# Kernel tuning notes

Measured on AMD Instinct MI355X. Metric: run time of the kernel, lower is better.

## Reference

```python
import jax, jax.numpy as jnp
import numpy as np

DIM_EMB = 1024
DIM_K = 128
DIM_V = 128
BATCH = 4
SEQ = 4096

def setup_inputs() -> dict:
    key = jax.random.key(0)
    kx, kq, kk, kv = jax.random.split(key, 4)
    x = jax.random.normal(kx, (BATCH, SEQ, DIM_EMB), dtype=jnp.float32)
    Wq = jax.random.normal(kq, (DIM_EMB, DIM_K), dtype=jnp.float32) * (1.0 / np.sqrt(DIM_EMB))
    Wk = jax.random.normal(kk, (DIM_EMB, DIM_K), dtype=jnp.float32) * (1.0 / np.sqrt(DIM_EMB))
    Wv = jax.random.normal(kv, (DIM_EMB, DIM_V), dtype=jnp.float32) * (1.0 / np.sqrt(DIM_EMB))
    return {"x": x, "Wq": Wq, "Wk": Wk, "Wv": Wv}

def reference(x, Wq, Wk, Wv):
    # x: [b, s, e]; projections (torch Linear without bias -> x @ W)
    seq_len = x.shape[1]
    q = x @ Wq  # [b, s, dk]
    k = x @ Wk  # [b, s, dk]
    v = x @ Wv  # [b, s, dv]
    # NOTE: original scales by 1/sqrt(dim_emb), not 1/sqrt(dim_k)
    scale = 1.0 / np.sqrt(x.shape[-1])
    qk = jnp.einsum('bqd,bkd->bqk', q, k) * scale  # [b, s, s]
    causal = jnp.tril(jnp.ones((seq_len, seq_len), dtype=bool))
    masked_qk = jnp.where(causal, qk, -jnp.inf)
    att = jax.nn.softmax(masked_qk, axis=-1)  # dropout p=0.0 -> identity
    return att @ v  # [b, s, dv]
```

## Files before the change

### kernel.cpp

```cpp
#include <hip/hip_runtime.h>

typedef __attribute__((ext_vector_type(8))) short s8v;
typedef __attribute__((ext_vector_type(4))) short s4v;
typedef __attribute__((ext_vector_type(4))) float f4v;

#define S_ 4096
#define E_ 1024
#define D_ 128

__device__ __forceinline__ unsigned short f2bf(float f) {
  unsigned int u = __float_as_uint(f);
  return (unsigned short)((u + 0x7FFFu + ((u >> 16) & 1u)) >> 16);
}

__device__ __forceinline__ unsigned int cvtpk(float lo, float hi) {
  unsigned int r;
  asm("v_cvt_pk_bf16_f32 %0, %1, %2" : "=v"(r) : "v"(lo), "v"(hi));
  return r;
}

__device__ __forceinline__ void gload16(const void* g, void* l) {
  __builtin_amdgcn_global_load_lds(
      (const __attribute__((address_space(1))) unsigned int*)g,
      (__attribute__((address_space(3))) unsigned int*)l, 16, 0, 0);
}

__device__ __forceinline__ int slot_off(int s) { return s * (3840 - 256 * s); }

__global__ __launch_bounds__(256) void prep_kernel(
    const float* __restrict__ Wq, const float* __restrict__ Wk,
    const float* __restrict__ Wv, unsigned short* __restrict__ Wt) {
  __shared__ unsigned short T[64][72];
  const int w = blockIdx.x;
  const int p = w >> 5, bx = w & 31;
  const float* W = (p == 0) ? Wq : (p == 1) ? Wk : Wv;
  const int k0 = (bx >> 1) * 64;
  const int n0 = (bx & 1) * 64;
  const int t = threadIdx.x, rr = t >> 4, c4 = (t & 15) * 4;
#pragma unroll
  for (int i = 0; i < 4; ++i) {
    int kr = i * 16 + rr;
    float4 ww = *reinterpret_cast<const float4*>(W + (size_t)(k0 + kr) * D_ + n0 + c4);
    T[c4 + 0][kr] = f2bf(ww.x); T[c4 + 1][kr] = f2bf(ww.y);
    T[c4 + 2][kr] = f2bf(ww.z); T[c4 + 3][kr] = f2bf(ww.w);
  }
  __syncthreads();
#pragma unroll
  for (int i = 0; i < 4; ++i) {
    int n = i * 16 + rr;
    s4v v;
    v[0] = (short)T[n][c4]; v[1] = (short)T[n][c4 + 1];
    v[2] = (short)T[n][c4 + 2]; v[3] = (short)T[n][c4 + 3];
    *reinterpret_cast<s4v*>(Wt + (size_t)(p * D_ + n0 + n) * E_ + k0 + c4) = v;
  }
}

__global__ __launch_bounds__(256, 3) void proj_kernel(
    const float* __restrict__ x, const unsigned short* __restrict__ Wt,
    unsigned short* __restrict__ Qb, unsigned short* __restrict__ Kb,
    unsigned short* __restrict__ VT) {
  __shared__ __align__(16) unsigned short As[2][128 * 64];
  __shared__ __align__(16) unsigned short Bs[2][64 * 64];
  const int bid = blockIdx.x;
  const int cls = bid & 7, j = bid >> 3;
  const int m0 = (cls * 16 + j / 6) * 128, ng = j % 6;
  const int t = threadIdx.x;
  const int wv = t >> 6, lane = t & 63, quad = lane >> 4, l16 = lane & 15;
  const int wr = wv >> 1, wc = wv & 1;

  f4v acc[4][2];
  const f4v fz = {0.f, 0.f, 0.f, 0.f};
#pragma unroll
  for (int i = 0; i < 4; ++i)
#pragma unroll
    for (int k = 0; k < 2; ++k) acc[i][k] = fz;

  const int ar = t >> 1, khalf = t & 1;
  const float* xg = x + (size_t)(m0 + ar) * E_ + khalf * 32;

  const int lrow = lane >> 3;
  const int scb = ((lane & 7) ^ lrow) * 16;
  const char* bSrc = (const char*)(Wt + (size_t)(ng * 64 + wv * 16 + lrow) * E_) + scb;

  const int xm = (l16 & 7) * 16;

  float4 xa[8];
#pragma unroll
  for (int m = 0; m < 8; ++m) xa[m] = *reinterpret_cast<const float4*>(xg + 4 * m);
#pragma unroll
  for (int i = 0; i < 2; ++i)
    gload16(bSrc + (size_t)(i * 8 * E_) * 2, (char*)Bs[0] + wv * 2048 + i * 1024);

  int buf = 0;
  for (int kk = 0; kk < E_; kk += 64, buf ^= 1) {
#pragma unroll
    for (int j2 = 0; j2 < 4; ++j2) {
      union { unsigned int u[4]; s8v v; } gv;
      gv.u[0] = cvtpk(xa[2 * j2].x, xa[2 * j2].y);
      gv.u[1] = cvtpk(xa[2 * j2].z, xa[2 * j2].w);
      gv.u[2] = cvtpk(xa[2 * j2 + 1].x, xa[2 * j2 + 1].y);
      gv.u[3] = cvtpk(xa[2 * j2 + 1].z, xa[2 * j2 + 1].w);
      const int g = khalf * 4 + j2;
      *reinterpret_cast<s8v*>((char*)As[buf] + ar * 128 + ((g ^ (ar & 7)) * 16)) = gv.v;
    }
    __syncthreads();
    if (kk + 64 < E_) {
#pragma unroll
      for (int m = 0; m < 8; ++m)
        xa[m] = *reinterpret_cast<const float4*>(xg + kk + 64 + 4 * m);
#pragma unroll
      for (int i = 0; i < 2; ++i)
        gload16(bSrc + (size_t)(i * 8 * E_ + kk + 64) * 2,
                (char*)Bs[buf ^ 1] + wv * 2048 + i * 1024);
    }
    const char* Ab = (const char*)As[buf] + (wr * 64 + l16) * 128;
    const char* Bb = (const char*)Bs[buf] + (wc * 32 + l16) * 128;
#pragma unroll
    for (int ks = 0; ks < 2; ++ks) {
      const int co = (ks * 64 + quad * 16) ^ xm;
      s8v af[4], bf[2];
#pragma unroll
      for (int rt = 0; rt < 4; ++rt)
        af[rt] = *reinterpret_cast<const s8v*>(Ab + rt * 2048 + co);
#pragma unroll
      for (int ct = 0; ct < 2; ++ct)
        bf[ct] = *reinterpret_cast<const s8v*>(Bb + ct * 2048 + co);
#pragma unroll
      for (int rt = 0; rt < 4; ++rt)
#pragma unroll
        for (int ct = 0; ct < 2; ++ct)
          acc[rt][ct] = __builtin_amdgcn_mfma_f32_16x16x32_bf16(
              af[rt], bf[ct], acc[rt][ct], 0, 0, 0);
    }
  }

  const int p = ng >> 1, n0 = (ng & 1) * 64;
  if (p < 2) {
    unsigned short* dst = p ? Kb : Qb;
#pragma unroll
    for (int rt = 0; rt < 4; ++rt)
#pragma unroll
      for (int ct = 0; ct < 2; ++ct)
#pragma unroll
        for (int r = 0; r < 4; ++r)
          dst[(size_t)(m0 + wr * 64 + rt * 16 + quad * 4 + r) * D_ +
              n0 + wc * 32 + ct * 16 + l16] = f2bf(acc[rt][ct][r]);
  } else {
    const int b = m0 >> 12;
    const int s0 = (m0 & (S_ - 1)) + wr * 64;
#pragma unroll
    for (int rt = 0; rt < 4; ++rt)
#pragma unroll
      for (int ct = 0; ct < 2; ++ct) {
        s4v v;
        v[0] = (short)f2bf(acc[rt][ct][0]); v[1] = (short)f2bf(acc[rt][ct][1]);
        v[2] = (short)f2bf(acc[rt][ct][2]); v[3] = (short)f2bf(acc[rt][ct][3]);
        *reinterpret_cast<s4v*>(
            VT + ((size_t)b * D_ + n0 + wc * 32 + ct * 16 + l16) * S_ + s0 +
            rt * 16 + quad * 4) = v;
      }
  }
}

__global__ __launch_bounds__(256, 5) void flash_kernel(
    const unsigned short* __restrict__ Qb, const unsigned short* __restrict__ Kb,
    const unsigned short* __restrict__ VT, float* __restrict__ Op,
    float* __restrict__ Lp) {
  __shared__ __align__(16) unsigned short KS[64 * 128];
  __shared__ __align__(16) unsigned short VS[128 * 64];
  const int id = blockIdx.x;
  const int xcd = id & 7;
  const int b = xcd >> 1;
  const int sub = 287 - ((id >> 3) * 2 + (xcd & 1));
  int g = 0;
#pragma unroll
  for (int gg = 0; gg < 7; ++gg)
    if (sub >= 4 * (gg + 1) * (gg + 2)) g = gg + 1;
  const int off = sub - 4 * g * (g + 1);
  const int qt = 8 * g + off / (g + 1);
  const int s = off % (g + 1);
  const int q0 = qt * 64;
  const int klo = s * 512;
  const int khi = min((s + 1) * 512, (qt + 1) * 64);

  const int t = threadIdx.x;
  const int wv = t >> 6, lane = t & 63, quad = lane >> 4, l16 = lane & 15;
  const int qrow0 = q0 + wv * 16;
  const float SCL2 = 0.03125f * 1.44269504088896340736f;

  const unsigned short* Kbb = Kb + (size_t)b * S_ * D_;
  const unsigned short* Vbb = VT + (size_t)b * D_ * S_;

  s8v Qf[4];
#pragma unroll
  for (int ks = 0; ks < 4; ++ks)
    Qf[ks] = *reinterpret_cast<const s8v*>(
        Qb + ((size_t)b * S_ + qrow0 + l16) * D_ + ks * 32 + quad * 8);

  f4v O[8];
  const f4v fz = {0.f, 0.f, 0.f, 0.f};
#pragma unroll
  for (int nt = 0; nt < 8; ++nt) O[nt] = fz;
  float lt = 0.f;

  for (int k0 = klo; k0 < khi; k0 += 64) {
    __syncthreads();
#pragma unroll
    for (int i = 0; i < 4; ++i) {
      const int ci = wv * 4 + i;
      const int kr = ci * 4 + (lane >> 4);
      const int sg = (kr & 3) | (((((kr >> 3) & 1) + 2 * (kr >> 4)) & 3) << 2);
      gload16(Kbb + (size_t)(k0 + kr) * D_ + (((lane & 15) ^ sg) * 8),
              (char*)KS + ci * 1024);
      const int dv = ci * 8 + (lane >> 3);
      gload16(Vbb + (size_t)dv * S_ + k0 + (((lane & 7) ^ (dv & 7)) * 8),
              (char*)VS + ci * 1024);
    }
    __syncthreads();

    if (k0 <= qrow0 + 15) {
      f4v St[2][2];
#pragma unroll
      for (int c = 0; c < 2; ++c)
#pragma unroll
        for (int s2 = 0; s2 < 2; ++s2) St[c][s2] = fz;
      __builtin_amdgcn_s_setprio(1);
#pragma unroll
      for (int ks = 0; ks < 4; ++ks)
#pragma unroll
        for (int c = 0; c < 2; ++c)
#pragma unroll
          for (int s2 = 0; s2 < 2; ++s2) {
            const int row = c * 32 + ((l16 >> 2) << 3) + s2 * 4 + (l16 & 3);
            s8v kf = *reinterpret_cast<const s8v*>(
                KS + row * 128 + (((ks * 4 + quad) ^ l16) * 8));
            St[c][s2] = __builtin_amdgcn_mfma_f32_16x16x32_bf16(
                kf, Qf[ks], St[c][s2], 0, 0, 0);
          }
      __builtin_amdgcn_s_setprio(0);
      const bool full = (k0 + 63 <= qrow0);
      s8v pf[2];
#pragma unroll
      for (int c = 0; c < 2; ++c) {
        float e[8];
        float ladd = 0.f;
#pragma unroll
        for (int s2 = 0; s2 < 2; ++s2)
#pragma unroll
          for (int r = 0; r < 4; ++r) {
            float ev = exp2f(St[c][s2][r] * SCL2);
            if (!full) {
              int key = k0 + c * 32 + quad * 8 + s2 * 4 + r;
              if (key > qrow0 + l16) ev = 0.f;
            }
            e[s2 * 4 + r] = ev;
            ladd += ev;
          }
        lt += ladd;
        union { unsigned int u[4]; s8v v; } P;
        P.u[0] = cvtpk(e[0], e[1]); P.u[1] = cvtpk(e[2], e[3]);
        P.u[2] = cvtpk(e[4], e[5]); P.u[3] = cvtpk(e[6], e[7]);
        pf[c] = P.v;
      }
      __builtin_amdgcn_s_setprio(1);
#pragma unroll
      for (int c = 0; c < 2; ++c)
#pragma unroll
        for (int nt = 0; nt < 8; ++nt) {
          s8v vf = *reinterpret_cast<const s8v*>(
              (const char*)VS + (nt * 16 + l16) * 128 +
              (((c * 4 + quad) ^ (l16 & 7)) * 16));
          O[nt] = __builtin_amdgcn_mfma_f32_16x16x32_bf16(
              pf[c], vf, O[nt], 0, 0, 0);
        }
      __builtin_amdgcn_s_setprio(0);
    }
  }

  lt += __shfl_xor(lt, 16);
  lt += __shfl_xor(lt, 32);
  const int soff = slot_off(s);
#pragma unroll
  for (int nt = 0; nt < 8; ++nt)
#pragma unroll
    for (int r = 0; r < 4; ++r)
      Op[((size_t)(qrow0 + quad * 4 + r + soff) * 4 + b) * D_ + nt * 16 + l16] =
          O[nt][r];
  if (lane < 16) Lp[(size_t)(qrow0 + l16 + soff) * 4 + b] = lt;
}

__global__ __launch_bounds__(256) void norm_kernel(
    const float* __restrict__ Op, const float* __restrict__ Lp,
    float* __restrict__ out) {
  const int idx = blockIdx.x * 256 + threadIdx.x;
  const int rowg = idx >> 5, d4 = idx & 31;
  const int b = rowg >> 12, row = rowg & 4095;
  const int g = row >> 9;
  float ax = 0.f, ay = 0.f, az = 0.f, aw = 0.f, L = 0.f;
  for (int s = 0; s <= g; ++s) {
    const size_t pr = (size_t)(row + slot_off(s)) * 4 + b;
    float4 o = reinterpret_cast<const float4*>(Op + pr * D_)[d4];
    ax += o.x; ay += o.y; az += o.z; aw += o.w;
    L += Lp[pr];
  }
  float4 r;
  const float inv = 1.f / L;
  r.x = ax * inv; r.y = ay * inv; r.z = az * inv; r.w = aw * inv;
  reinterpret_cast<float4*>(out)[idx] = r;
}

extern "C" void kernel_launch(void* const* d_in, const int* in_sizes, int n_in,
                              void* d_out, int out_size, void* d_ws, size_t ws_size,
                              hipStream_t stream) {
  const float* x = (const float*)d_in[0];
  const float* Wq = (const float*)d_in[1];
  const float* Wk = (const float*)d_in[2];
  const float* Wv = (const float*)d_in[3];
  float* out = (float*)d_out;

  char* ws = (char*)d_ws;
  unsigned short* Qb = (unsigned short*)ws;
  unsigned short* Kb = (unsigned short*)(ws + (((size_t)4) << 20));
  unsigned short* VT = (unsigned short*)(ws + (((size_t)8) << 20));
  unsigned short* Wt = (unsigned short*)(ws + (((size_t)12) << 20));
  float* Op = (float*)(ws + (((size_t)13) << 20));
  float* Lp = (float*)(ws + (((size_t)50) << 20));

  prep_kernel<<<96, 256, 0, stream>>>(Wq, Wk, Wv, Wt);
  proj_kernel<<<768, 256, 0, stream>>>(x, Wt, Qb, Kb, VT);
  flash_kernel<<<1152, 256, 0, stream>>>(Qb, Kb, VT, Op, Lp);
  norm_kernel<<<2048, 256, 0, stream>>>(Op, Lp, out);
}
```

Before: 204.5 us.

## Load fp32 x directly to LDS in projection; register-prefetch K/V in flash kernel

The projection kernel now streams fp32 x tiles straight into LDS with direct global-to-LDS loads and converts to bf16 while reading MFMA fragments. This replaces the register-staged, double-buffered bf16 A tile with a single fp32 buffer, and occupancy hints rise to 4 blocks per CU. The flash kernel swaps direct global-to-LDS K/V loads for register prefetching of the next tile during compute, and raises its occupancy hint to 8. The projection loses its double buffering, so load latency is hidden only by other resident blocks, and the flash kernel now uses more registers for the prefetch.

New measurement: 186.6 us. 8.8% less time.

```diff
diff --git a/kernel.cpp b/kernel.cpp
--- a/kernel.cpp
+++ b/kernel.cpp
@@ -55,12 +55,12 @@
   }
 }
 
-__global__ __launch_bounds__(256, 3) void proj_kernel(
+__global__ __launch_bounds__(256, 4) void proj_kernel(
     const float* __restrict__ x, const unsigned short* __restrict__ Wt,
     unsigned short* __restrict__ Qb, unsigned short* __restrict__ Kb,
     unsigned short* __restrict__ VT) {
-  __shared__ __align__(16) unsigned short As[2][128 * 64];
-  __shared__ __align__(16) unsigned short Bs[2][64 * 64];
+  __shared__ __align__(16) float Asf[128 * 64];
+  __shared__ __align__(16) unsigned short Bsb[64 * 64];
   const int bid = blockIdx.x;
   const int cls = bid & 7, j = bid >> 3;
   const int m0 = (cls * 16 + j / 6) * 128, ng = j % 6;
@@ -75,53 +75,42 @@
 #pragma unroll
     for (int k = 0; k < 2; ++k) acc[i][k] = fz;
 
-  const int ar = t >> 1, khalf = t & 1;
-  const float* xg = x + (size_t)(m0 + ar) * E_ + khalf * 32;
-
+  const char* aSrc0 =
+      (const char*)(x + (size_t)(m0 + wv * 32 + (lane >> 4)) * E_);
   const int lrow = lane >> 3;
   const int scb = ((lane & 7) ^ lrow) * 16;
   const char* bSrc = (const char*)(Wt + (size_t)(ng * 64 + wv * 16 + lrow) * E_) + scb;
 
-  const int xm = (l16 & 7) * 16;
-
-  float4 xa[8];
-#pragma unroll
-  for (int m = 0; m < 8; ++m) xa[m] = *reinterpret_cast<const float4*>(xg + 4 * m);
-#pragma unroll
-  for (int i = 0; i < 2; ++i)
-    gload16(bSrc + (size_t)(i * 8 * E_) * 2, (char*)Bs[0] + wv * 2048 + i * 1024);
-
-  int buf = 0;
-  for (int kk = 0; kk < E_; kk += 64, buf ^= 1) {
-#pragma unroll
-    for (int j2 = 0; j2 < 4; ++j2) {
-      union { unsigned int u[4]; s8v v; } gv;
-      gv.u[0] = cvtpk(xa[2 * j2].x, xa[2 * j2].y);
-      gv.u[1] = cvtpk(xa[2 * j2].z, xa[2 * j2].w);
-      gv.u[2] = cvtpk(xa[2 * j2 + 1].x, xa[2 * j2 + 1].y);
-      gv.u[3] = cvtpk(xa[2 * j2 + 1].z, xa[2 * j2 + 1].w);
-      const int g = khalf * 4 + j2;
-      *reinterpret_cast<s8v*>((char*)As[buf] + ar * 128 + ((g ^ (ar & 7)) * 16)) = gv.v;
-    }
+  const char* Ab = (const char*)Asf + (size_t)(wr * 64 + l16) * 256;
+  const char* Bb = (const char*)Bsb + (wc * 32 + l16) * 128;
+
+  for (int kk = 0; kk < E_; kk += 64) {
+#pragma unroll
+    for (int i = 0; i < 8; ++i) {
+      const int gsrc = (lane & 15) ^ ((i * 4 + (lane >> 4)) & 15);
+      gload16(aSrc0 + (size_t)i * 16384 + kk * 4 + gsrc * 16,
+              (char*)Asf + wv * 8192 + i * 1024);
+    }
+#pragma unroll
+    for (int i = 0; i < 2; ++i)
+      gload16(bSrc + (size_t)(i * 8 * E_ + kk) * 2, (char*)Bsb + wv * 2048 + i * 1024);
     __syncthreads();
-    if (kk + 64 < E_) {
-#pragma unroll
-      for (int m = 0; m < 8; ++m)
-        xa[m] = *reinterpret_cast<const float4*>(xg + kk + 64 + 4 * m);
-#pragma unroll
-      for (int i = 0; i < 2; ++i)
-        gload16(bSrc + (size_t)(i * 8 * E_ + kk + 64) * 2,
-                (char*)Bs[buf ^ 1] + wv * 2048 + i * 1024);
-    }
-    const char* Ab = (const char*)As[buf] + (wr * 64 + l16) * 128;
-    const char* Bb = (const char*)Bs[buf] + (wc * 32 + l16) * 128;
 #pragma unroll
     for (int ks = 0; ks < 2; ++ks) {
-      const int co = (ks * 64 + quad * 16) ^ xm;
       s8v af[4], bf[2];
-#pragma unroll
-      for (int rt = 0; rt < 4; ++rt)
-        af[rt] = *reinterpret_cast<const s8v*>(Ab + rt * 2048 + co);
+      const int g0 = ks * 8 + quad * 2;
+#pragma unroll
+      for (int rt = 0; rt < 4; ++rt) {
+        float4 a0 = *reinterpret_cast<const float4*>(
+            Ab + rt * 4096 + ((g0 ^ l16) << 4));
+        float4 a1 = *reinterpret_cast<const float4*>(
+            Ab + rt * 4096 + (((g0 + 1) ^ l16) << 4));
+        union { unsigned int u[4]; s8v v; } c;
+        c.u[0] = cvtpk(a0.x, a0.y); c.u[1] = cvtpk(a0.z, a0.w);
+        c.u[2] = cvtpk(a1.x, a1.y); c.u[3] = cvtpk(a1.z, a1.w);
+        af[rt] = c.v;
+      }
+      const int co = (ks * 64 + quad * 16) ^ ((l16 & 7) * 16);
 #pragma unroll
       for (int ct = 0; ct < 2; ++ct)
         bf[ct] = *reinterpret_cast<const s8v*>(Bb + ct * 2048 + co);
@@ -132,6 +121,7 @@
           acc[rt][ct] = __builtin_amdgcn_mfma_f32_16x16x32_bf16(
               af[rt], bf[ct], acc[rt][ct], 0, 0, 0);
     }
+    __syncthreads();
   }
 
   const int p = ng >> 1, n0 = (ng & 1) * 64;
@@ -162,7 +152,7 @@
   }
 }
 
-__global__ __launch_bounds__(256, 5) void flash_kernel(
+__global__ __launch_bounds__(256, 8) void flash_kernel(
     const unsigned short* __restrict__ Qb, const unsigned short* __restrict__ Kb,
     const unsigned short* __restrict__ VT, float* __restrict__ Op,
     float* __restrict__ Lp) {
@@ -203,20 +193,38 @@
   for (int nt = 0; nt < 8; ++nt) O[nt] = fz;
   float lt = 0.f;
 
+  const int krow = t >> 4, kgb = t & 15;
+  const int vrow = t >> 1, vgb = (t & 1) * 4;
+
+  s8v kr[4], vr[4];
+#pragma unroll
+  for (int i = 0; i < 4; ++i) {
+    kr[i] = *reinterpret_cast<const s8v*>(
+        Kbb + (size_t)(klo + krow + 16 * i) * D_ + kgb * 8);
+    vr[i] = *reinterpret_cast<const s8v*>(
+        Vbb + (size_t)vrow * S_ + klo + (vgb + i) * 8);
+  }
+
   for (int k0 = klo; k0 < khi; k0 += 64) {
     __syncthreads();
 #pragma unroll
     for (int i = 0; i < 4; ++i) {
-      const int ci = wv * 4 + i;
-      const int kr = ci * 4 + (lane >> 4);
-      const int sg = (kr & 3) | (((((kr >> 3) & 1) + 2 * (kr >> 4)) & 3) << 2);
-      gload16(Kbb + (size_t)(k0 + kr) * D_ + (((lane & 15) ^ sg) * 8),
-              (char*)KS + ci * 1024);
-      const int dv = ci * 8 + (lane >> 3);
-      gload16(Vbb + (size_t)dv * S_ + k0 + (((lane & 7) ^ (dv & 7)) * 8),
-              (char*)VS + ci * 1024);
+      const int r = krow + 16 * i;
+      const int sig = (krow & 3) | ((((krow >> 3) + 2 * i) & 3) << 2);
+      *reinterpret_cast<s8v*>(KS + r * 128 + ((kgb ^ sig) * 8)) = kr[i];
+      *reinterpret_cast<s8v*>(
+          (char*)VS + vrow * 128 + (((vgb + i) ^ (vrow & 7)) << 4)) = vr[i];
     }
     __syncthreads();
+    if (k0 + 64 < khi) {
+#pragma unroll
+      for (int i = 0; i < 4; ++i) {
+        kr[i] = *reinterpret_cast<const s8v*>(
+            Kbb + (size_t)(k0 + 64 + krow + 16 * i) * D_ + kgb * 8);
+        vr[i] = *reinterpret_cast<const s8v*>(
+            Vbb + (size_t)vrow * S_ + k0 + 64 + (vgb + i) * 8);
+      }
+    }
 
     if (k0 <= qrow0 + 15) {
       f4v St[2][2];
@@ -269,7 +277,7 @@
         for (int nt = 0; nt < 8; ++nt) {
           s8v vf = *reinterpret_cast<const s8v*>(
               (const char*)VS + (nt * 16 + l16) * 128 +
-              (((c * 4 + quad) ^ (l16 & 7)) * 16));
+              ((((c * 4 + quad)) ^ (l16 & 7)) << 4));
           O[nt] = __builtin_amdgcn_mfma_f32_16x16x32_bf16(
               pf[c], vf, O[nt], 0, 0, 0);
         }
```
